# Optimization experiments

Measured on AMD Instinct MI355X. Metric: run time of the kernel, lower is better.

Reference implementation:

```python
import jax, jax.numpy as jnp
import numpy as np

B, T, I, H, OUT = 256, 512, 64, 512, 1

def _init_lstm(key, in_sz, hid):
    k = 1.0 / np.sqrt(hid)
    ks = jax.random.split(key, 4)
    W_ih = jax.random.uniform(ks[0], (4 * hid, in_sz), jnp.float32, -k, k)
    W_hh = jax.random.uniform(ks[1], (4 * hid, hid), jnp.float32, -k, k)
    b_ih = jax.random.uniform(ks[2], (4 * hid,), jnp.float32, -k, k)
    b_hh = jax.random.uniform(ks[3], (4 * hid,), jnp.float32, -k, k)
    return W_ih, W_hh, b_ih, b_hh

def setup_inputs() -> dict:
    key = jax.random.key(0)
    kx, ky, k0, k1, kl = jax.random.split(key, 5)
    x = jax.random.normal(kx, (B, T, I), jnp.float32)
    y = jax.random.normal(ky, (B, OUT), jnp.float32)
    W_ih0, W_hh0, b_ih0, b_hh0 = _init_lstm(k0, I, H)
    W_ih1, W_hh1, b_ih1, b_hh1 = _init_lstm(k1, H, H)
    kl1, kl2 = jax.random.split(kl)
    kk = 1.0 / np.sqrt(H)
    W_lin = jax.random.uniform(kl1, (OUT, H), jnp.float32, -kk, kk)
    b_lin = jax.random.uniform(kl2, (OUT,), jnp.float32, -kk, kk)
    return {"x": x, "y": y,
            "W_ih0": W_ih0, "W_hh0": W_hh0, "b_ih0": b_ih0, "b_hh0": b_hh0,
            "W_ih1": W_ih1, "W_hh1": W_hh1, "b_ih1": b_ih1, "b_hh1": b_hh1,
            "W_lin": W_lin, "b_lin": b_lin}

def _lstm_cell(x_t, h, c, W_ih, W_hh, b_ih, b_hh):
    # PyTorch LSTMCell gate order: i, f, g, o
    gates = x_t @ W_ih.T + b_ih + h @ W_hh.T + b_hh  # [B, 4H]
    i_g, f_g, g_g, o_g = jnp.split(gates, 4, axis=-1)
    c_new = jax.nn.sigmoid(f_g) * c + jax.nn.sigmoid(i_g) * jnp.tanh(g_g)
    h_new = jax.nn.sigmoid(o_g) * jnp.tanh(c_new)
    return h_new, c_new

def reference(x, y, W_ih0, W_hh0, b_ih0, b_hh0, W_ih1, W_hh1, b_ih1, b_hh1, W_lin, b_lin):
    b = x.shape[0]
    hid = W_hh0.shape[1]
    zeros = jnp.zeros((b, hid), x.dtype)
    init = (zeros, zeros, zeros, zeros)  # h0, c0, h1, c1

    def step(carry, x_t):
        h0, c0, h1, c1 = carry
        h0, c0 = _lstm_cell(x_t, h0, c0, W_ih0, W_hh0, b_ih0, b_hh0)
        h1, c1 = _lstm_cell(h0, h1, c1, W_ih1, W_hh1, b_ih1, b_hh1)
        # dropout_prob=0.0 -> dropout is identity
        return (h0, c0, h1, c1), None

    (h0, c0, h1, c1), _ = jax.lax.scan(step, init, jnp.swapaxes(x, 0, 1))
    out = h1 @ W_lin.T + b_lin  # [B, OUT]
    loss = jnp.mean((out - y) ** 2)
    return out, loss
```

## Files before the change

kernel.cpp:

```cpp
#include <hip/hip_runtime.h>

#define TDIM 512
#define BDIM 256
#define IDIM 64
#define HDIM 512

typedef short bf16x8 __attribute__((ext_vector_type(8)));
typedef float f32x4  __attribute__((ext_vector_type(4)));

__device__ __forceinline__ unsigned short f2bf(float f) {
  union { float f; unsigned u; } v; v.f = f;
  return (unsigned short)((v.u + 0x7fffu + ((v.u >> 16) & 1u)) >> 16);
}

__device__ __forceinline__ bf16x8 load8f_bf16(const float* p) {
  float4 a = *(const float4*)p;
  float4 b = *(const float4*)(p + 4);
  bf16x8 r;
  r[0] = (short)f2bf(a.x); r[1] = (short)f2bf(a.y);
  r[2] = (short)f2bf(a.z); r[3] = (short)f2bf(a.w);
  r[4] = (short)f2bf(b.x); r[5] = (short)f2bf(b.y);
  r[6] = (short)f2bf(b.z); r[7] = (short)f2bf(b.w);
  return r;
}

__device__ __forceinline__ bf16x8 load_h16(const unsigned short* p) {
  union { unsigned long long u[2]; bf16x8 v; } r;
  r.u[0] = __hip_atomic_load((const unsigned long long*)p,
                             __ATOMIC_RELAXED, __HIP_MEMORY_SCOPE_AGENT);
  r.u[1] = __hip_atomic_load((const unsigned long long*)(p + 4),
                             __ATOMIC_RELAXED, __HIP_MEMORY_SCOPE_AGENT);
  return r.v;
}

__device__ __forceinline__ float sigm(float x)   { return 1.0f / (1.0f + __expf(-x)); }
__device__ __forceinline__ float tanh_f(float x) { return 2.0f / (1.0f + __expf(-2.0f * x)) - 1.0f; }

__device__ __forceinline__ void wait32(const int* base, int tgt) {
  const int* p = base + (threadIdx.x & 31);
  while (true) {
    int v = __hip_atomic_load(p, __ATOMIC_RELAXED, __HIP_MEMORY_SCOPE_AGENT);
    if (__all(v >= tgt)) break;
    __builtin_amdgcn_s_sleep(2);
  }
  asm volatile("" ::: "memory");
}

__global__ __launch_bounds__(256, 1)
void lstm_persist(const float* __restrict__ x,
                  const float* __restrict__ Wih0, const float* __restrict__ Whh0,
                  const float* __restrict__ bih0, const float* __restrict__ bhh0,
                  const float* __restrict__ Wih1, const float* __restrict__ Whh1,
                  const float* __restrict__ bih1, const float* __restrict__ bhh1,
                  unsigned short* __restrict__ h0b, unsigned short* __restrict__ h1b,
                  float* __restrict__ h1f, int* __restrict__ flags)
{
  const int tid  = threadIdx.x;
  const int w    = tid >> 6;
  const int lane = tid & 63;
  const int lrow = lane & 15;
  const int lk8  = (lane >> 4) << 3;
  const int bid  = blockIdx.x;
  const int bi   = bid & 7;
  const int hj   = bid >> 3;

  int* words = flags + bi * 32;

  __shared__ float part0[4 * 64 * 36];
  __shared__ float part1[4 * 64 * 36];

  bf16x8 bwx[4];
  bf16x8 bw0h[4][4];
  bf16x8 bw1a[4][4];
  bf16x8 bw1b[4][4];
  #pragma unroll
  for (int g = 0; g < 4; ++g) {
    int j = g * 512 + hj * 16 + lrow;
    if (w < 2) bwx[g] = load8f_bf16(Wih0 + (size_t)j * 64 + (w * 32 + lk8));
    else       { bf16x8 z = {0,0,0,0,0,0,0,0}; bwx[g] = z; }
    #pragma unroll
    for (int s = 0; s < 4; ++s) {
      int ch = w + 4 * s;
      bw0h[s][g] = load8f_bf16(Whh0 + (size_t)j * 512 + (ch * 32 + lk8));
      bw1a[s][g] = load8f_bf16(Wih1 + (size_t)j * 512 + (ch * 32 + lk8));
      bw1b[s][g] = load8f_bf16(Whh1 + (size_t)j * 512 + (ch * 32 + lk8));
    }
  }

  const int hp  = tid & 7;
  const int r   = tid >> 3;
  const int jc0 = hj * 16 + 2 * hp;
  const int grow = bi * 32 + r;
  float bia0[2][4], bia1[2][4];
  #pragma unroll
  for (int cc = 0; cc < 2; ++cc)
    #pragma unroll
    for (int g = 0; g < 4; ++g) {
      bia0[cc][g] = bih0[g * 512 + jc0 + cc] + bhh0[g * 512 + jc0 + cc];
      bia1[cc][g] = bih1[g * 512 + jc0 + cc] + bhh1[g * 512 + jc0 + cc];
    }

  float c0s[2] = {0.f, 0.f}, c1s[2] = {0.f, 0.f};

  const size_t HB = (size_t)BDIM * HDIM;
  const int r0w = ((lane >> 4) << 2);

  #pragma unroll 1
  for (int t = 0; t <= TDIM; ++t) {
    f32x4 acc0[2][4], acc1[2][4];
    #pragma unroll
    for (int m = 0; m < 2; ++m)
      #pragma unroll
      for (int g = 0; g < 4; ++g) {
        f32x4 z = {0.f,0.f,0.f,0.f}; acc0[m][g] = z; acc1[m][g] = z;
      }

    if (t < TDIM && w < 2) {
      bf16x8 a[2];
      #pragma unroll
      for (int m = 0; m < 2; ++m)
        a[m] = load8f_bf16(x + ((size_t)(bi * 32 + m * 16 + lrow) * TDIM + t) * IDIM + (w * 32 + lk8));
      #pragma unroll
      for (int m = 0; m < 2; ++m)
        #pragma unroll
        for (int g = 0; g < 4; ++g)
          acc0[m][g] = __builtin_amdgcn_mfma_f32_16x16x32_bf16(a[m], bwx[g], acc0[m][g], 0, 0, 0);
    }

    wait32(words, t);

    const unsigned short* h0p = h0b + (size_t)((t + 1) & 1) * HB;
    const unsigned short* h1p = h1b + (size_t)(t & 1) * HB;

    bf16x8 ah0[4][2], ah1[4][2];
    #pragma unroll
    for (int s = 0; s < 4; ++s) {
      int ch = w + 4 * s;
      #pragma unroll
      for (int m = 0; m < 2; ++m) {
        size_t row = (size_t)(bi * 32 + m * 16 + lrow) * HDIM;
        ah0[s][m] = load_h16(h0p + row + (ch * 32 + lk8));
        ah1[s][m] = load_h16(h1p + row + (ch * 32 + lk8));
      }
    }

    if (t < TDIM) {
      #pragma unroll
      for (int s = 0; s < 4; ++s)
        #pragma unroll
        for (int m = 0; m < 2; ++m)
          #pragma unroll
          for (int g = 0; g < 4; ++g)
            acc0[m][g] = __builtin_amdgcn_mfma_f32_16x16x32_bf16(ah0[s][m], bw0h[s][g], acc0[m][g], 0, 0, 0);
    }
    if (t >= 1) {
      #pragma unroll
      for (int s = 0; s < 4; ++s)
        #pragma unroll
        for (int m = 0; m < 2; ++m)
          #pragma unroll
          for (int g = 0; g < 4; ++g) {
            acc1[m][g] = __builtin_amdgcn_mfma_f32_16x16x32_bf16(ah0[s][m], bw1a[s][g], acc1[m][g], 0, 0, 0);
            acc1[m][g] = __builtin_amdgcn_mfma_f32_16x16x32_bf16(ah1[s][m], bw1b[s][g], acc1[m][g], 0, 0, 0);
          }
    }

    if (t < TDIM) {
      #pragma unroll
      for (int m = 0; m < 2; ++m)
        #pragma unroll
        for (int g = 0; g < 4; ++g)
          *(f32x4*)&part0[(w * 64 + g * 16 + lrow) * 36 + m * 16 + r0w] = acc0[m][g];
    }
    if (t >= 1) {
      #pragma unroll
      for (int m = 0; m < 2; ++m)
        #pragma unroll
        for (int g = 0; g < 4; ++g)
          *(f32x4*)&part1[(w * 64 + g * 16 + lrow) * 36 + m * 16 + r0w] = acc1[m][g];
    }
    __syncthreads();

    if (t < TDIM) {
      unsigned short* h0w = h0b + (size_t)(t & 1) * HB;
      float hv[2];
      #pragma unroll
      for (int cc = 0; cc < 2; ++cc) {
        int hc = 2 * hp + cc;
        float gv[4];
        #pragma unroll
        for (int g = 0; g < 4; ++g) {
          float sum = bia0[cc][g];
          #pragma unroll
          for (int w4 = 0; w4 < 4; ++w4)
            sum += part0[(w4 * 64 + g * 16 + hc) * 36 + r];
          gv[g] = sum;
        }
        float ig = sigm(gv[0]), fg = sigm(gv[1]), gg = tanh_f(gv[2]), og = sigm(gv[3]);
        c0s[cc] = fg * c0s[cc] + ig * gg;
        hv[cc] = og * tanh_f(c0s[cc]);
      }
      unsigned packed = (unsigned)f2bf(hv[0]) | ((unsigned)f2bf(hv[1]) << 16);
      __hip_atomic_store((unsigned*)(h0w + (size_t)grow * HDIM + jc0), packed,
                         __ATOMIC_RELAXED, __HIP_MEMORY_SCOPE_AGENT);
    }
    if (t >= 1) {
      unsigned short* h1w = h1b + (size_t)((t + 1) & 1) * HB;
      float hv[2];
      #pragma unroll
      for (int cc = 0; cc < 2; ++cc) {
        int hc = 2 * hp + cc;
        float gv[4];
        #pragma unroll
        for (int g = 0; g < 4; ++g) {
          float sum = bia1[cc][g];
          #pragma unroll
          for (int w4 = 0; w4 < 4; ++w4)
            sum += part1[(w4 * 64 + g * 16 + hc) * 36 + r];
          gv[g] = sum;
        }
        float ig = sigm(gv[0]), fg = sigm(gv[1]), gg = tanh_f(gv[2]), og = sigm(gv[3]);
        c1s[cc] = fg * c1s[cc] + ig * gg;
        hv[cc] = og * tanh_f(c1s[cc]);
      }
      unsigned packed = (unsigned)f2bf(hv[0]) | ((unsigned)f2bf(hv[1]) << 16);
      __hip_atomic_store((unsigned*)(h1w + (size_t)grow * HDIM + jc0), packed,
                         __ATOMIC_RELAXED, __HIP_MEMORY_SCOPE_AGENT);
      if (t == TDIM) {
        float2 o; o.x = hv[0]; o.y = hv[1];
        *(float2*)(h1f + (size_t)grow * HDIM + jc0) = o;
      }
    }

    asm volatile("s_waitcnt vmcnt(0)" ::: "memory");
    __syncthreads();
    if (tid == 0)
      __hip_atomic_store(&words[hj], t + 1, __ATOMIC_RELAXED, __HIP_MEMORY_SCOPE_AGENT);
  }
}

__global__ void head_k(const float* __restrict__ h1f, const float* __restrict__ Wlin,
                       const float* __restrict__ blin, const float* __restrict__ y,
                       float* __restrict__ dout)
{
  __shared__ float red[256];
  int b = threadIdx.x;
  const float4* hp = (const float4*)(h1f + (size_t)b * HDIM);
  const float4* wp = (const float4*)Wlin;
  float acc = 0.f;
  #pragma unroll 8
  for (int i = 0; i < HDIM / 4; ++i) {
    float4 h4 = hp[i]; float4 w4 = wp[i];
    acc += h4.x * w4.x + h4.y * w4.y + h4.z * w4.z + h4.w * w4.w;
  }
  float o = acc + blin[0];
  dout[b] = o;
  float d = o - y[b];
  red[b] = d * d;
  __syncthreads();
  for (int off = 128; off > 0; off >>= 1) {
    if (b < off) red[b] += red[b + off];
    __syncthreads();
  }
  if (b == 0) dout[256] = red[0] * (1.0f / 256.0f);
}

extern "C" void kernel_launch(void* const* d_in, const int* in_sizes, int n_in,
                              void* d_out, int out_size, void* d_ws, size_t ws_size,
                              hipStream_t stream)
{
  const float* x    = (const float*)d_in[0];
  const float* y    = (const float*)d_in[1];
  const float* Wih0 = (const float*)d_in[2];
  const float* Whh0 = (const float*)d_in[3];
  const float* bih0 = (const float*)d_in[4];
  const float* bhh0 = (const float*)d_in[5];
  const float* Wih1 = (const float*)d_in[6];
  const float* Whh1 = (const float*)d_in[7];
  const float* bih1 = (const float*)d_in[8];
  const float* bhh1 = (const float*)d_in[9];
  const float* Wlin = (const float*)d_in[10];
  const float* blin = (const float*)d_in[11];

  char* ws = (char*)d_ws;
  unsigned short* h0b = (unsigned short*)ws;
  unsigned short* h1b = (unsigned short*)(ws + 524288);
  int*   flags = (int*)(ws + 1048576);
  float* h1f   = (float*)(ws + 1048576 + 4096);

  hipMemsetAsync(d_ws, 0, 1048576 + 4096, stream);

  hipLaunchKernelGGL(lstm_persist, dim3(256), dim3(256), 0, stream,
                     x, Wih0, Whh0, bih0, bhh0, Wih1, Whh1, bih1, bhh1,
                     h0b, h1b, h1f, flags);
  hipLaunchKernelGGL(head_k, dim3(1), dim3(256), 0, stream,
                     h1f, Wlin, blin, y, (float*)d_out);
}
```

Before: 3.656 ms.

## Split each batch group into two 16-row halves with separate flag groups

Each block now processes its 32 batch rows as two 16-row sub-steps, each with its own set of 32 sync flags, so one half can be published while the other is still being computed. Gate epilogue work is split across threads by layer (first 128 threads do layer 0, the rest layer 1) instead of every thread doing both layers serially. The flag polling is done by one wave followed by a block barrier. This adds an extra barrier round per sub-step and doubles the number of flag-wait points per time step. The flags array must hold twice as many groups as before.

```diff
diff --git a/kernel.cpp b/kernel.cpp
--- a/kernel.cpp
+++ b/kernel.cpp
@@ -4,6 +4,7 @@
 #define BDIM 256
 #define IDIM 64
 #define HDIM 512
+#define PSTR 20
 
 typedef short bf16x8 __attribute__((ext_vector_type(8)));
 typedef float f32x4  __attribute__((ext_vector_type(4)));
@@ -35,16 +36,6 @@
 
 __device__ __forceinline__ float sigm(float x)   { return 1.0f / (1.0f + __expf(-x)); }
 __device__ __forceinline__ float tanh_f(float x) { return 2.0f / (1.0f + __expf(-2.0f * x)) - 1.0f; }
-
-__device__ __forceinline__ void wait32(const int* base, int tgt) {
-  const int* p = base + (threadIdx.x & 31);
-  while (true) {
-    int v = __hip_atomic_load(p, __ATOMIC_RELAXED, __HIP_MEMORY_SCOPE_AGENT);
-    if (__all(v >= tgt)) break;
-    __builtin_amdgcn_s_sleep(2);
-  }
-  asm volatile("" ::: "memory");
-}
 
 __global__ __launch_bounds__(256, 1)
 void lstm_persist(const float* __restrict__ x,
@@ -64,10 +55,7 @@
   const int bi   = bid & 7;
   const int hj   = bid >> 3;
 
-  int* words = flags + bi * 32;
-
-  __shared__ float part0[4 * 64 * 36];
-  __shared__ float part1[4 * 64 * 36];
+  __shared__ float part[2][2][4 * 64 * PSTR];
 
   bf16x8 bwx[4];
   bf16x8 bw0h[4][4];
@@ -87,155 +75,140 @@
     }
   }
 
-  const int hp  = tid & 7;
-  const int r   = tid >> 3;
-  const int jc0 = hj * 16 + 2 * hp;
-  const int grow = bi * 32 + r;
-  float bia0[2][4], bia1[2][4];
+  const int elay = tid >> 7;
+  const int hp   = tid & 7;
+  const int er   = (tid >> 3) & 15;
+  const int jc0  = hj * 16 + 2 * hp;
+  const float* bihp = elay ? bih1 : bih0;
+  const float* bhhp = elay ? bhh1 : bhh0;
+  float bia[2][4];
   #pragma unroll
   for (int cc = 0; cc < 2; ++cc)
     #pragma unroll
-    for (int g = 0; g < 4; ++g) {
-      bia0[cc][g] = bih0[g * 512 + jc0 + cc] + bhh0[g * 512 + jc0 + cc];
-      bia1[cc][g] = bih1[g * 512 + jc0 + cc] + bhh1[g * 512 + jc0 + cc];
-    }
-
-  float c0s[2] = {0.f, 0.f}, c1s[2] = {0.f, 0.f};
+    for (int g = 0; g < 4; ++g)
+      bia[cc][g] = bihp[g * 512 + jc0 + cc] + bhhp[g * 512 + jc0 + cc];
+
+  float cst[2][2] = {{0.f, 0.f}, {0.f, 0.f}};
 
   const size_t HB = (size_t)BDIM * HDIM;
-  const int r0w = ((lane >> 4) << 2);
+  const int r0w = (lane >> 4) << 2;
 
   #pragma unroll 1
   for (int t = 0; t <= TDIM; ++t) {
-    f32x4 acc0[2][4], acc1[2][4];
-    #pragma unroll
-    for (int m = 0; m < 2; ++m)
+    bf16x8 xf[2];
+    #pragma unroll
+    for (int ss = 0; ss < 2; ++ss) { bf16x8 z = {0,0,0,0,0,0,0,0}; xf[ss] = z; }
+    if (t < TDIM && w < 2) {
+      #pragma unroll
+      for (int ss = 0; ss < 2; ++ss)
+        xf[ss] = load8f_bf16(x + ((size_t)(bi * 32 + ss * 16 + lrow) * TDIM + t) * IDIM + (w * 32 + lk8));
+    }
+
+    #pragma unroll
+    for (int ss = 0; ss < 2; ++ss) {
+      const int gbase = bi * 32 + ss * 16;
+      int* words = flags + (bi * 2 + ss) * 32;
+
+      f32x4 acc0[4], acc1[4];
       #pragma unroll
       for (int g = 0; g < 4; ++g) {
-        f32x4 z = {0.f,0.f,0.f,0.f}; acc0[m][g] = z; acc1[m][g] = z;
-      }
-
-    if (t < TDIM && w < 2) {
-      bf16x8 a[2];
+        f32x4 z = {0.f,0.f,0.f,0.f}; acc0[g] = z; acc1[g] = z;
+      }
+
+      if (t < TDIM && w < 2) {
+        #pragma unroll
+        for (int g = 0; g < 4; ++g)
+          acc0[g] = __builtin_amdgcn_mfma_f32_16x16x32_bf16(xf[ss], bwx[g], acc0[g], 0, 0, 0);
+      }
+
+      if (w == 0) {
+        const int* p = words + (lane & 31);
+        while (true) {
+          int v = __hip_atomic_load(p, __ATOMIC_RELAXED, __HIP_MEMORY_SCOPE_AGENT);
+          if (__all(v >= t)) break;
+          __builtin_amdgcn_s_sleep(2);
+        }
+      }
+      __syncthreads();
+      asm volatile("" ::: "memory");
+
+      const unsigned short* h0p = h0b + (size_t)((t + 1) & 1) * HB;
+      const unsigned short* h1p = h1b + (size_t)(t & 1) * HB;
+
+      bf16x8 ah0[4], ah1[4];
+      const size_t hrow = (size_t)(gbase + lrow) * HDIM;
       #pragma unroll
-      for (int m = 0; m < 2; ++m)
-        a[m] = load8f_bf16(x + ((size_t)(bi * 32 + m * 16 + lrow) * TDIM + t) * IDIM + (w * 32 + lk8));
-      #pragma unroll
-      for (int m = 0; m < 2; ++m)
-        #pragma unroll
-        for (int g = 0; g < 4; ++g)
-          acc0[m][g] = __builtin_amdgcn_mfma_f32_16x16x32_bf16(a[m], bwx[g], acc0[m][g], 0, 0, 0);
-    }
-
-    wait32(words, t);
-
-    const unsigned short* h0p = h0b + (size_t)((t + 1) & 1) * HB;
-    const unsigned short* h1p = h1b + (size_t)(t & 1) * HB;
-
-    bf16x8 ah0[4][2], ah1[4][2];
-    #pragma unroll
-    for (int s = 0; s < 4; ++s) {
-      int ch = w + 4 * s;
-      #pragma unroll
-      for (int m = 0; m < 2; ++m) {
-        size_t row = (size_t)(bi * 32 + m * 16 + lrow) * HDIM;
-        ah0[s][m] = load_h16(h0p + row + (ch * 32 + lk8));
-        ah1[s][m] = load_h16(h1p + row + (ch * 32 + lk8));
-      }
-    }
-
-    if (t < TDIM) {
-      #pragma unroll
-      for (int s = 0; s < 4; ++s)
-        #pragma unroll
-        for (int m = 0; m < 2; ++m)
+      for (int s = 0; s < 4; ++s) {
+        int ch = w + 4 * s;
+        ah0[s] = load_h16(h0p + hrow + (ch * 32 + lk8));
+        ah1[s] = load_h16(h1p + hrow + (ch * 32 + lk8));
+      }
+
+      if (t < TDIM) {
+        #pragma unroll
+        for (int s = 0; s < 4; ++s)
           #pragma unroll
           for (int g = 0; g < 4; ++g)
-            acc0[m][g] = __builtin_amdgcn_mfma_f32_16x16x32_bf16(ah0[s][m], bw0h[s][g], acc0[m][g], 0, 0, 0);
-    }
-    if (t >= 1) {
-      #pragma unroll
-      for (int s = 0; s < 4; ++s)
-        #pragma unroll
-        for (int m = 0; m < 2; ++m)
+            acc0[g] = __builtin_amdgcn_mfma_f32_16x16x32_bf16(ah0[s], bw0h[s][g], acc0[g], 0, 0, 0);
+      }
+      if (t >= 1) {
+        #pragma unroll
+        for (int s = 0; s < 4; ++s)
           #pragma unroll
           for (int g = 0; g < 4; ++g) {
-            acc1[m][g] = __builtin_amdgcn_mfma_f32_16x16x32_bf16(ah0[s][m], bw1a[s][g], acc1[m][g], 0, 0, 0);
-            acc1[m][g] = __builtin_amdgcn_mfma_f32_16x16x32_bf16(ah1[s][m], bw1b[s][g], acc1[m][g], 0, 0, 0);
+            acc1[g] = __builtin_amdgcn_mfma_f32_16x16x32_bf16(ah0[s], bw1a[s][g], acc1[g], 0, 0, 0);
+            acc1[g] = __builtin_amdgcn_mfma_f32_16x16x32_bf16(ah1[s], bw1b[s][g], acc1[g], 0, 0, 0);
           }
+      }
+
+      if (t < TDIM) {
+        #pragma unroll
+        for (int g = 0; g < 4; ++g)
+          *(f32x4*)&part[ss][0][(w * 64 + g * 16 + lrow) * PSTR + r0w] = acc0[g];
+      }
+      if (t >= 1) {
+        #pragma unroll
+        for (int g = 0; g < 4; ++g)
+          *(f32x4*)&part[ss][1][(w * 64 + g * 16 + lrow) * PSTR + r0w] = acc1[g];
+      }
+      __syncthreads();
+
+      const bool act = elay ? (t >= 1) : (t < TDIM);
+      if (act) {
+        const float* pp = &part[ss][elay][0];
+        float hv[2];
+        #pragma unroll
+        for (int cc = 0; cc < 2; ++cc) {
+          int hc = 2 * hp + cc;
+          float gv[4];
+          #pragma unroll
+          for (int g = 0; g < 4; ++g) {
+            float sum = bia[cc][g];
+            #pragma unroll
+            for (int w4 = 0; w4 < 4; ++w4)
+              sum += pp[(w4 * 64 + g * 16 + hc) * PSTR + er];
+            gv[g] = sum;
+          }
+          float ig = sigm(gv[0]), fg = sigm(gv[1]), gg = tanh_f(gv[2]), og = sigm(gv[3]);
+          cst[ss][cc] = fg * cst[ss][cc] + ig * gg;
+          hv[cc] = og * tanh_f(cst[ss][cc]);
+        }
+        unsigned packed = (unsigned)f2bf(hv[0]) | ((unsigned)f2bf(hv[1]) << 16);
+        unsigned short* hw = elay ? (h1b + (size_t)((t + 1) & 1) * HB)
+                                  : (h0b + (size_t)(t & 1) * HB);
+        __hip_atomic_store((unsigned*)(hw + (size_t)(gbase + er) * HDIM + jc0), packed,
+                           __ATOMIC_RELAXED, __HIP_MEMORY_SCOPE_AGENT);
+        if (elay && t == TDIM) {
+          float2 o; o.x = hv[0]; o.y = hv[1];
+          *(float2*)(h1f + (size_t)(gbase + er) * HDIM + jc0) = o;
+        }
+      }
+
+      asm volatile("s_waitcnt vmcnt(0)" ::: "memory");
+      __syncthreads();
+      if (tid == 0)
+        __hip_atomic_store(&words[hj], t + 1, __ATOMIC_RELAXED, __HIP_MEMORY_SCOPE_AGENT);
     }
-
-    if (t < TDIM) {
-      #pragma unroll
-      for (int m = 0; m < 2; ++m)
-        #pragma unroll
-        for (int g = 0; g < 4; ++g)
-          *(f32x4*)&part0[(w * 64 + g * 16 + lrow) * 36 + m * 16 + r0w] = acc0[m][g];
-    }
-    if (t >= 1) {
-      #pragma unroll
-      for (int m = 0; m < 2; ++m)
-        #pragma unroll
-        for (int g = 0; g < 4; ++g)
-          *(f32x4*)&part1[(w * 64 + g * 16 + lrow) * 36 + m * 16 + r0w] = acc1[m][g];
-    }
-    __syncthreads();
-
-    if (t < TDIM) {
-      unsigned short* h0w = h0b + (size_t)(t & 1) * HB;
-      float hv[2];
-      #pragma unroll
-      for (int cc = 0; cc < 2; ++cc) {
-        int hc = 2 * hp + cc;
-        float gv[4];
-        #pragma unroll
-        for (int g = 0; g < 4; ++g) {
-          float sum = bia0[cc][g];
-          #pragma unroll
-          for (int w4 = 0; w4 < 4; ++w4)
-            sum += part0[(w4 * 64 + g * 16 + hc) * 36 + r];
-          gv[g] = sum;
-        }
-        float ig = sigm(gv[0]), fg = sigm(gv[1]), gg = tanh_f(gv[2]), og = sigm(gv[3]);
-        c0s[cc] = fg * c0s[cc] + ig * gg;
-        hv[cc] = og * tanh_f(c0s[cc]);
-      }
-      unsigned packed = (unsigned)f2bf(hv[0]) | ((unsigned)f2bf(hv[1]) << 16);
-      __hip_atomic_store((unsigned*)(h0w + (size_t)grow * HDIM + jc0), packed,
-                         __ATOMIC_RELAXED, __HIP_MEMORY_SCOPE_AGENT);
-    }
-    if (t >= 1) {
-      unsigned short* h1w = h1b + (size_t)((t + 1) & 1) * HB;
-      float hv[2];
-      #pragma unroll
-      for (int cc = 0; cc < 2; ++cc) {
-        int hc = 2 * hp + cc;
-        float gv[4];
-        #pragma unroll
-        for (int g = 0; g < 4; ++g) {
-          float sum = bia1[cc][g];
-          #pragma unroll
-          for (int w4 = 0; w4 < 4; ++w4)
-            sum += part1[(w4 * 64 + g * 16 + hc) * 36 + r];
-          gv[g] = sum;
-        }
-        float ig = sigm(gv[0]), fg = sigm(gv[1]), gg = tanh_f(gv[2]), og = sigm(gv[3]);
-        c1s[cc] = fg * c1s[cc] + ig * gg;
-        hv[cc] = og * tanh_f(c1s[cc]);
-      }
-      unsigned packed = (unsigned)f2bf(hv[0]) | ((unsigned)f2bf(hv[1]) << 16);
-      __hip_atomic_store((unsigned*)(h1w + (size_t)grow * HDIM + jc0), packed,
-                         __ATOMIC_RELAXED, __HIP_MEMORY_SCOPE_AGENT);
-      if (t == TDIM) {
-        float2 o; o.x = hv[0]; o.y = hv[1];
-        *(float2*)(h1f + (size_t)grow * HDIM + jc0) = o;
-      }
-    }
-
-    asm volatile("s_waitcnt vmcnt(0)" ::: "memory");
-    __syncthreads();
-    if (tid == 0)
-      __hip_atomic_store(&words[hj], t + 1, __ATOMIC_RELAXED, __HIP_MEMORY_SCOPE_AGENT);
   }
 }
 
```

New measurement: 4.322 ms. 18.2% more time.

## Split per-step barrier into separate layer-0 and layer-1 flag phases

Applied to the files above, without the earlier changes.

Replaces the single per-timestep inter-block flag barrier with two flag sets, one for layer 0 and one for layer 1. Layer 0's h0 is published and its flag raised before layer 1's matmul runs, so dependent blocks can begin earlier. Polling is now done by one wave followed by a block barrier, and the two LDS partial buffers are merged into one. In exchange there are two global synchronisations per step instead of one, with extra __syncthreads, and the flag array must now hold 512 ints.

```diff
diff --git a/kernel.cpp b/kernel.cpp
--- a/kernel.cpp
+++ b/kernel.cpp
@@ -35,16 +35,6 @@
 
 __device__ __forceinline__ float sigm(float x)   { return 1.0f / (1.0f + __expf(-x)); }
 __device__ __forceinline__ float tanh_f(float x) { return 2.0f / (1.0f + __expf(-2.0f * x)) - 1.0f; }
-
-__device__ __forceinline__ void wait32(const int* base, int tgt) {
-  const int* p = base + (threadIdx.x & 31);
-  while (true) {
-    int v = __hip_atomic_load(p, __ATOMIC_RELAXED, __HIP_MEMORY_SCOPE_AGENT);
-    if (__all(v >= tgt)) break;
-    __builtin_amdgcn_s_sleep(2);
-  }
-  asm volatile("" ::: "memory");
-}
 
 __global__ __launch_bounds__(256, 1)
 void lstm_persist(const float* __restrict__ x,
@@ -64,10 +54,10 @@
   const int bi   = bid & 7;
   const int hj   = bid >> 3;
 
-  int* words = flags + bi * 32;
-
-  __shared__ float part0[4 * 64 * 36];
-  __shared__ float part1[4 * 64 * 36];
+  int* words0 = flags + bi * 32;
+  int* words1 = flags + 256 + bi * 32;
+
+  __shared__ float part[4 * 64 * 36];
 
   bf16x8 bwx[4];
   bf16x8 bw0h[4][4];
@@ -107,13 +97,11 @@
 
   #pragma unroll 1
   for (int t = 0; t <= TDIM; ++t) {
-    f32x4 acc0[2][4], acc1[2][4];
+    f32x4 acc[2][4];
     #pragma unroll
     for (int m = 0; m < 2; ++m)
       #pragma unroll
-      for (int g = 0; g < 4; ++g) {
-        f32x4 z = {0.f,0.f,0.f,0.f}; acc0[m][g] = z; acc1[m][g] = z;
-      }
+      for (int g = 0; g < 4; ++g) { f32x4 z = {0.f,0.f,0.f,0.f}; acc[m][g] = z; }
 
     if (t < TDIM && w < 2) {
       bf16x8 a[2];
@@ -124,24 +112,28 @@
       for (int m = 0; m < 2; ++m)
         #pragma unroll
         for (int g = 0; g < 4; ++g)
-          acc0[m][g] = __builtin_amdgcn_mfma_f32_16x16x32_bf16(a[m], bwx[g], acc0[m][g], 0, 0, 0);
-    }
-
-    wait32(words, t);
+          acc[m][g] = __builtin_amdgcn_mfma_f32_16x16x32_bf16(a[m], bwx[g], acc[m][g], 0, 0, 0);
+    }
+
+    if (w == 0) {
+      const int* p = words0 + (lane & 31);
+      while (true) {
+        int v = __hip_atomic_load(p, __ATOMIC_RELAXED, __HIP_MEMORY_SCOPE_AGENT);
+        if (__all(v >= t)) break;
+        __builtin_amdgcn_s_sleep(2);
+      }
+    }
+    __syncthreads();
+    asm volatile("" ::: "memory");
 
     const unsigned short* h0p = h0b + (size_t)((t + 1) & 1) * HB;
-    const unsigned short* h1p = h1b + (size_t)(t & 1) * HB;
-
-    bf16x8 ah0[4][2], ah1[4][2];
+    bf16x8 ah0[4][2];
     #pragma unroll
     for (int s = 0; s < 4; ++s) {
       int ch = w + 4 * s;
       #pragma unroll
-      for (int m = 0; m < 2; ++m) {
-        size_t row = (size_t)(bi * 32 + m * 16 + lrow) * HDIM;
-        ah0[s][m] = load_h16(h0p + row + (ch * 32 + lk8));
-        ah1[s][m] = load_h16(h1p + row + (ch * 32 + lk8));
-      }
+      for (int m = 0; m < 2; ++m)
+        ah0[s][m] = load_h16(h0p + (size_t)(bi * 32 + m * 16 + lrow) * HDIM + (ch * 32 + lk8));
     }
 
     if (t < TDIM) {
@@ -151,33 +143,12 @@
         for (int m = 0; m < 2; ++m)
           #pragma unroll
           for (int g = 0; g < 4; ++g)
-            acc0[m][g] = __builtin_amdgcn_mfma_f32_16x16x32_bf16(ah0[s][m], bw0h[s][g], acc0[m][g], 0, 0, 0);
-    }
-    if (t >= 1) {
-      #pragma unroll
-      for (int s = 0; s < 4; ++s)
-        #pragma unroll
-        for (int m = 0; m < 2; ++m)
-          #pragma unroll
-          for (int g = 0; g < 4; ++g) {
-            acc1[m][g] = __builtin_amdgcn_mfma_f32_16x16x32_bf16(ah0[s][m], bw1a[s][g], acc1[m][g], 0, 0, 0);
-            acc1[m][g] = __builtin_amdgcn_mfma_f32_16x16x32_bf16(ah1[s][m], bw1b[s][g], acc1[m][g], 0, 0, 0);
-          }
-    }
-
-    if (t < TDIM) {
+            acc[m][g] = __builtin_amdgcn_mfma_f32_16x16x32_bf16(ah0[s][m], bw0h[s][g], acc[m][g], 0, 0, 0);
       #pragma unroll
       for (int m = 0; m < 2; ++m)
         #pragma unroll
         for (int g = 0; g < 4; ++g)
-          *(f32x4*)&part0[(w * 64 + g * 16 + lrow) * 36 + m * 16 + r0w] = acc0[m][g];
-    }
-    if (t >= 1) {
-      #pragma unroll
-      for (int m = 0; m < 2; ++m)
-        #pragma unroll
-        for (int g = 0; g < 4; ++g)
-          *(f32x4*)&part1[(w * 64 + g * 16 + lrow) * 36 + m * 16 + r0w] = acc1[m][g];
+          *(f32x4*)&part[(w * 64 + g * 16 + lrow) * 36 + m * 16 + r0w] = acc[m][g];
     }
     __syncthreads();
 
@@ -193,7 +164,7 @@
           float sum = bia0[cc][g];
           #pragma unroll
           for (int w4 = 0; w4 < 4; ++w4)
-            sum += part0[(w4 * 64 + g * 16 + hc) * 36 + r];
+            sum += part[(w4 * 64 + g * 16 + hc) * 36 + r];
           gv[g] = sum;
         }
         float ig = sigm(gv[0]), fg = sigm(gv[1]), gg = tanh_f(gv[2]), og = sigm(gv[3]);
@@ -204,6 +175,53 @@
       __hip_atomic_store((unsigned*)(h0w + (size_t)grow * HDIM + jc0), packed,
                          __ATOMIC_RELAXED, __HIP_MEMORY_SCOPE_AGENT);
     }
+    asm volatile("s_waitcnt vmcnt(0)" ::: "memory");
+    __syncthreads();
+    if (tid == 0)
+      __hip_atomic_store(&words0[hj], t + 1, __ATOMIC_RELAXED, __HIP_MEMORY_SCOPE_AGENT);
+
+    if (w == 0) {
+      const int* p = words1 + (lane & 31);
+      while (true) {
+        int v = __hip_atomic_load(p, __ATOMIC_RELAXED, __HIP_MEMORY_SCOPE_AGENT);
+        if (__all(v >= t)) break;
+        __builtin_amdgcn_s_sleep(2);
+      }
+    }
+    __syncthreads();
+    asm volatile("" ::: "memory");
+
+    if (t >= 1) {
+      const unsigned short* h1p = h1b + (size_t)(t & 1) * HB;
+      bf16x8 ah1[4][2];
+      #pragma unroll
+      for (int s = 0; s < 4; ++s) {
+        int ch = w + 4 * s;
+        #pragma unroll
+        for (int m = 0; m < 2; ++m)
+          ah1[s][m] = load_h16(h1p + (size_t)(bi * 32 + m * 16 + lrow) * HDIM + (ch * 32 + lk8));
+      }
+      #pragma unroll
+      for (int m = 0; m < 2; ++m)
+        #pragma unroll
+        for (int g = 0; g < 4; ++g) { f32x4 z = {0.f,0.f,0.f,0.f}; acc[m][g] = z; }
+      #pragma unroll
+      for (int s = 0; s < 4; ++s)
+        #pragma unroll
+        for (int m = 0; m < 2; ++m)
+          #pragma unroll
+          for (int g = 0; g < 4; ++g) {
+            acc[m][g] = __builtin_amdgcn_mfma_f32_16x16x32_bf16(ah0[s][m], bw1a[s][g], acc[m][g], 0, 0, 0);
+            acc[m][g] = __builtin_amdgcn_mfma_f32_16x16x32_bf16(ah1[s][m], bw1b[s][g], acc[m][g], 0, 0, 0);
+          }
+      #pragma unroll
+      for (int m = 0; m < 2; ++m)
+        #pragma unroll
+        for (int g = 0; g < 4; ++g)
+          *(f32x4*)&part[(w * 64 + g * 16 + lrow) * 36 + m * 16 + r0w] = acc[m][g];
+    }
+    __syncthreads();
+
     if (t >= 1) {
       unsigned short* h1w = h1b + (size_t)((t + 1) & 1) * HB;
       float hv[2];
@@ -216,7 +234,7 @@
           float sum = bia1[cc][g];
           #pragma unroll
           for (int w4 = 0; w4 < 4; ++w4)
-            sum += part1[(w4 * 64 + g * 16 + hc) * 36 + r];
+            sum += part[(w4 * 64 + g * 16 + hc) * 36 + r];
           gv[g] = sum;
         }
         float ig = sigm(gv[0]), fg = sigm(gv[1]), gg = tanh_f(gv[2]), og = sigm(gv[3]);
@@ -231,11 +249,10 @@
         *(float2*)(h1f + (size_t)grow * HDIM + jc0) = o;
       }
     }
-
     asm volatile("s_waitcnt vmcnt(0)" ::: "memory");
     __syncthreads();
     if (tid == 0)
-      __hip_atomic_store(&words[hj], t + 1, __ATOMIC_RELAXED, __HIP_MEMORY_SCOPE_AGENT);
+      __hip_atomic_store(&words1[hj], t + 1, __ATOMIC_RELAXED, __HIP_MEMORY_SCOPE_AGENT);
   }
 }
 
```

New measurement: 4.331 ms. 1.18x slower.
